# Performance work log

Hardware: AMD Instinct MI355X
Metric: run time of the kernel (lower is better)

The kernel has to match this reference:

```python
import jax, jax.numpy as jnp
import numpy as np

N = 100000   # nodes
C = 128      # in_channels
K = 32       # n_super_nodes
B = 16       # graphs in batch
TAU = 1.0
EPS = 1e-9
SPARSITY_W = 0.01
TEMPORAL_W = 0.1 * 5
COLLAPSE_W = 2.0


def setup_inputs() -> dict:
    key = jax.random.key(0)
    ks = jax.random.split(key, 8)
    x = jax.random.normal(ks[0], (N, C), dtype=jnp.float32)
    batch = jnp.sort(jax.random.randint(ks[1], (N,), 0, B)).astype(jnp.int64)
    pos = jax.random.normal(ks[2], (N, 2), dtype=jnp.float32)
    gumbel_u = jax.random.uniform(ks[3], (N, K), dtype=jnp.float32,
                                  minval=1e-6, maxval=1.0 - 1e-6)
    W1 = jax.random.normal(ks[4], (C, C), dtype=jnp.float32) / np.float32(np.sqrt(C))
    b1 = jnp.zeros((C,), jnp.float32)
    W2 = jax.random.normal(ks[5], (C, K), dtype=jnp.float32) / np.float32(np.sqrt(C))
    b2 = jnp.zeros((K,), jnp.float32)
    scaling = jnp.asarray(10.0, jnp.float32)
    active_mask = jnp.ones((K,), jnp.float32)
    return dict(x=x, batch=batch, pos=pos, gumbel_u=gumbel_u,
                W1=W1, b1=b1, W2=W2, b2=b2, scaling=scaling,
                active_mask=active_mask)


def reference(x, batch, pos, gumbel_u, W1, b1, W2, b2, scaling, active_mask):
    # assign MLP: Linear -> ReLU -> Linear, scaled
    h = jax.nn.relu(x @ W1 + b1)                      # [N, C]
    logits = (h @ W2 + b2) * scaling                  # [N, K]
    # eval-mode masking of inactive super-nodes (active_mask is a detached buffer)
    mask = jax.lax.stop_gradient(active_mask)[None, :]
    logits = jnp.where(mask == 0, -1e9, logits)
    # Gumbel-softmax (soft, hard=False) with explicit uniform noise
    g = -jnp.log(-jnp.log(gumbel_u + EPS) + EPS)
    s = jax.nn.softmax((logits + g) / TAU, axis=-1)   # [N, K]

    avg_s = s.mean(axis=0)                            # [K]
    entropy = -jnp.mean(jnp.sum(s * jnp.log(s + EPS), axis=1))
    uniform_p = 1.0 / K
    diversity = jnp.sum(uniform_p * jnp.log(uniform_p / (avg_s + EPS)))
    pruning = jnp.mean(jnp.abs(avg_s * (1.0 - active_mask)))
    sparsity = (jnp.sum(active_mask) / K) * SPARSITY_W
    temporal = jnp.asarray(0.0, s.dtype)  # prev_assignments=None

    # collapse prevention (common_losses approximation: normalized entropy
    # deficit + peak-mass penalty), scaled by collapse weight
    ent_avg = -jnp.sum(avg_s * jnp.log(avg_s + EPS))
    collapse = ((jnp.log(jnp.asarray(K, s.dtype)) - ent_avg)
                / jnp.log(jnp.asarray(K, s.dtype))
                + jax.nn.relu(jnp.max(avg_s) - 2.0 / K)) * COLLAPSE_W
    # balance (KL(avg_s || uniform))
    balance = jnp.sum(avg_s * jnp.log(avg_s * K + EPS))

    # spatial variance loss over column-normalized assignments
    s_sum = s.sum(axis=0, keepdims=True) + EPS        # [1, K]
    s_norm = s / s_sum                                # [N, K]
    mu = s_norm.T @ pos                               # [K, 2]
    pos_sq = jnp.sum(pos ** 2, axis=1, keepdims=True) # [N, 1]
    st_pos = s_norm.T @ pos                           # [K, 2]
    var = (s_norm.T @ pos_sq)[:, 0] - 2.0 * jnp.sum(mu * st_pos, axis=1) \
          + jnp.sum(mu ** 2, axis=1)
    spatial = var.mean()

    # per-graph super-node centroids via segment pooling
    sum_s_pos = jax.ops.segment_sum(pos[:, None, :] * s[:, :, None], batch,
                                    num_segments=B)   # [B, K, 2]
    sum_s = jax.ops.segment_sum(s, batch, num_segments=B)[:, :, None] + EPS
    super_node_mu = sum_s_pos / sum_s                 # [B, K, 2]

    # separation loss among centroids
    d = super_node_mu[:, :, None, :] - super_node_mu[:, None, :, :]
    dist_sq = jnp.sum(d ** 2, axis=-1)                # [B, K, K]
    eye = jnp.eye(K, dtype=s.dtype)[None]
    repulsion = 1.0 / (dist_sq + 1.0)
    separation = jnp.sum(repulsion * (1.0 - eye)) / (K * (K - 1) + EPS)

    # hierarchical pooling: out[b,k,c] = sum_{i in graph b} s[i,k] * x[i,c]
    x_expanded = x[:, None, :] * s[:, :, None]        # [N, K, C]
    out = jax.ops.segment_sum(x_expanded, batch, num_segments=B)  # [B, K, C]

    losses = jnp.stack([entropy, diversity, spatial, pruning, sparsity,
                        temporal * TEMPORAL_W, collapse, balance, separation])
    return out, s, super_node_mu, losses
```

## Files before the change

kernel.cpp:

```cpp
#include <hip/hip_runtime.h>
#include <math.h>

#define NN 100000
#define CC 128
#define KK 32
#define BG 16
#define EPSF 1e-9f

#define NTILES 1563

#define S_OFF 65536
#define MU_OFF 3265536
#define LOSS_OFF 3266560

#define WS_ENTARR 0
#define WS_STAT 2048
#define WS_FIRST 4096
#define WS_LAST 4112
#define WS_ZERO_FLOATS 4096

#define W1B_OFF_BYTES 16896
#define W2B_OFF_BYTES 49664
#define WS_PART_FLOAT 16384
#define WS_NEEDED_BYTES (65536ull + (unsigned long long)NTILES * 4096ull * 4ull)

typedef __attribute__((ext_vector_type(8))) _Float16 half8;
typedef __attribute__((ext_vector_type(4))) _Float16 half4v;
typedef __attribute__((ext_vector_type(4))) float float4v;

#define MFMAH(a, b, c) __builtin_amdgcn_mfma_f32_16x16x32_f16((a), (b), (c), 0, 0, 0)

__global__ __launch_bounds__(256) void k_prep(const float* __restrict__ W1,
                                              const float* __restrict__ W2,
                                              const int* __restrict__ batch,
                                              _Float16* __restrict__ wW1,
                                              _Float16* __restrict__ wW2,
                                              int* __restrict__ firstp,
                                              int* __restrict__ lastp,
                                              float* __restrict__ dout,
                                              float* __restrict__ ws) {
    int tid = blockIdx.x * 256 + threadIdx.x;

    float4 z4 = make_float4(0.f, 0.f, 0.f, 0.f);
#pragma unroll
    for (int i = 0; i < 4; ++i) ((float4*)dout)[tid + i * 4096] = z4;
    ws[tid] = 0.f;

    if (tid < 8 * 4 * 64) {
        int l = tid & 63, ks = (tid >> 6) & 3, nt = tid >> 8;
        int n = nt * 16 + (l & 15);
        int cb = ks * 32 + (l >> 4) * 8;
        half8 H;
#pragma unroll
        for (int j = 0; j < 8; ++j) H[j] = (_Float16)W1[(size_t)(cb + j) * CC + n];
        ((half8*)wW1)[(nt * 4 + ks) * 64 + l] = H;
    } else if (tid < 2048 + 512) {
        int t2 = tid - 2048;
        int l = t2 & 63, ks = (t2 >> 6) & 3, nt = t2 >> 8;
        int n = nt * 16 + (l & 15);
        int cb = ks * 32 + (l >> 4) * 8;
        half8 H;
#pragma unroll
        for (int j = 0; j < 8; ++j) H[j] = (_Float16)W2[(size_t)(cb + j) * KK + n];
        ((half8*)wW2)[(nt * 4 + ks) * 64 + l] = H;
    } else if (tid < 2560 + 16) {
        int b = tid - 2560;
        int lo = 0, hi = NN;
        while (lo < hi) { int mid = (lo + hi) >> 1; if (batch[mid] < b) lo = mid + 1; else hi = mid; }
        int lob = lo;
        lo = 0; hi = NN;
        while (lo < hi) { int mid = (lo + hi) >> 1; if (batch[mid] < b + 1) lo = mid + 1; else hi = mid; }
        int hib = (b == BG - 1) ? NTILES * 64 : lo;
        firstp[b] = (lob + 63) >> 6;
        lastp[b]  = (hib >> 6) - 1;
    }
}

__global__ __launch_bounds__(256, 4) void k_assign(
    const float* __restrict__ x, const int* __restrict__ batch,
    const float* __restrict__ pos, const float* __restrict__ gum,
    const float* __restrict__ b1, const float* __restrict__ b2,
    const float* __restrict__ scaling, const float* __restrict__ amask,
    const _Float16* __restrict__ wW1, const _Float16* __restrict__ wW2,
    float* __restrict__ dout, float* __restrict__ ws,
    float* __restrict__ part)
{
    __shared__ _Float16 xh[64][136];
    __shared__ _Float16 hb[64][136];
    __shared__ _Float16 st[32][72];
    __shared__ float lpx[64], lpy[64], lpsq[64];
    __shared__ int lbat[64];
    float* sbuf = (float*)&hb[0][0];

    const int t = threadIdx.x;
    const bool usep = (part != nullptr);
    const int orig = blockIdx.x;
    const int qq = NTILES >> 3, rr8 = NTILES & 7;
    const int xcd = orig & 7, sidx = orig >> 3;
    const int tile = (xcd < rr8 ? xcd * (qq + 1) : rr8 * (qq + 1) + (xcd - rr8) * qq) + sidx;
    const int n0 = tile * 64;

    const int l = t & 63;
    const int wv = __builtin_amdgcn_readfirstlane(t >> 6);
    const int li = l & 15;
    const int g16 = l >> 4;
    const int cc4 = (t & 31) * 4;
    const int nb = t >> 5;
    const int ca  = (2 * wv) * 16 + li;
    const int cb2 = (2 * wv + 1) * 16 + li;
    const int sk = t & 31, sch = t >> 5;

    const float scal = scaling[0];
    const float b2v0 = b2[li], b2v1 = b2[16 + li];
    const float am0 = amask[li], am1 = amask[16 + li];
    const float bv0 = b1[(2 * wv) * 16 + li];
    const float bv1 = b1[(2 * wv + 1) * 16 + li];

#pragma unroll
    for (int r = 0; r < 8; ++r) {
        int n = r * 8 + nb;
        int gn = n0 + n;
        float4 v = make_float4(0.f, 0.f, 0.f, 0.f);
        if (gn < NN) v = *(const float4*)(x + (size_t)gn * CC + cc4);
        *(half4v*)&xh[n][cc4] =
            (half4v){(_Float16)v.x, (_Float16)v.y, (_Float16)v.z, (_Float16)v.w};
    }
    if (t < 64) {
        int gn = n0 + t;
        float px = 0.f, py = 0.f; int bb = BG - 1;
        if (gn < NN) { px = pos[gn * 2]; py = pos[gn * 2 + 1]; bb = batch[gn]; }
        lpx[t] = px; lpy[t] = py; lpsq[t] = px * px + py * py; lbat[t] = bb;
    }

    float gu[8];
#pragma unroll
    for (int r2 = 0; r2 < 4; ++r2) {
        int gn = n0 + wv * 16 + g16 * 4 + r2;
        bool valid = gn < NN;
        gu[r2 * 2]     = valid ? gum[(size_t)gn * KK + li]      : 0.5f;
        gu[r2 * 2 + 1] = valid ? gum[(size_t)gn * KK + 16 + li] : 0.5f;
    }
    __syncthreads();

    float4v acc[4][2];
#pragma unroll
    for (int mt = 0; mt < 4; ++mt) {
        acc[mt][0] = (float4v){0.f, 0.f, 0.f, 0.f};
        acc[mt][1] = (float4v){0.f, 0.f, 0.f, 0.f};
    }
    const half8* W1B = (const half8*)wW1;
#pragma unroll
    for (int ks = 0; ks < 4; ++ks) {
        half8 bh0 = W1B[((2 * wv    ) * 4 + ks) * 64 + l];
        half8 bh1 = W1B[((2 * wv + 1) * 4 + ks) * 64 + l];
#pragma unroll
        for (int mt = 0; mt < 4; ++mt) {
            half8 ah = *(const half8*)&xh[mt * 16 + li][ks * 32 + g16 * 8];
            acc[mt][0] = MFMAH(ah, bh0, acc[mt][0]);
            acc[mt][1] = MFMAH(ah, bh1, acc[mt][1]);
        }
    }

#pragma unroll
    for (int mt = 0; mt < 4; ++mt) {
#pragma unroll
        for (int r2 = 0; r2 < 4; ++r2) {
            int row = mt * 16 + g16 * 4 + r2;
            hb[row][(2 * wv) * 16 + li]     = (_Float16)fmaxf(acc[mt][0][r2] + bv0, 0.f);
            hb[row][(2 * wv + 1) * 16 + li] = (_Float16)fmaxf(acc[mt][1][r2] + bv1, 0.f);
        }
    }
    __syncthreads();

    float4v acc2[2];
    acc2[0] = (float4v){0.f, 0.f, 0.f, 0.f};
    acc2[1] = (float4v){0.f, 0.f, 0.f, 0.f};
    const half8* W2B = (const half8*)wW2;
#pragma unroll
    for (int ks = 0; ks < 4; ++ks) {
        half8 ah = *(const half8*)&hb[wv * 16 + li][ks * 32 + g16 * 8];
        acc2[0] = MFMAH(ah, W2B[(0 * 4 + ks) * 64 + l], acc2[0]);
        acc2[1] = MFMAH(ah, W2B[(1 * 4 + ks) * 64 + l], acc2[1]);
    }

    float ep_acc = 0.f;
    float sr0[4], sr1[4];
#pragma unroll
    for (int r2 = 0; r2 < 4; ++r2) {
        int m = wv * 16 + g16 * 4 + r2;
        int gn = n0 + m;
        bool valid = gn < NN;
        float lg0 = (acc2[0][r2] + b2v0) * scal; if (am0 == 0.f) lg0 = -1e9f;
        float lg1 = (acc2[1][r2] + b2v1) * scal; if (am1 == 0.f) lg1 = -1e9f;
        float z0 = lg0 - __logf(-__logf(gu[r2 * 2] + EPSF) + EPSF);
        float z1 = lg1 - __logf(-__logf(gu[r2 * 2 + 1] + EPSF) + EPSF);
        float e0 = __expf(z0), e1 = __expf(z1);
        float sm = e0 + e1;
        sm += __shfl_xor(sm, 1);
        sm += __shfl_xor(sm, 2);
        sm += __shfl_xor(sm, 4);
        sm += __shfl_xor(sm, 8);
        float inv = 1.f / sm;
        float s0 = e0 * inv, s1 = e1 * inv;
        if (!valid) { s0 = 0.f; s1 = 0.f; }
        sr0[r2] = s0; sr1[r2] = s1;
        st[li][m] = (_Float16)s0;
        st[16 + li][m] = (_Float16)s1;
        ep_acc += s0 * __logf(s0 + EPSF) + s1 * __logf(s1 + EPSF);
    }
    __syncthreads();

    ep_acc += __shfl_xor(ep_acc, 1);
    ep_acc += __shfl_xor(ep_acc, 2);
    ep_acc += __shfl_xor(ep_acc, 4);
    ep_acc += __shfl_xor(ep_acc, 8);
    ep_acc += __shfl_xor(ep_acc, 16);
    ep_acc += __shfl_xor(ep_acc, 32);
    if (l == 0) sbuf[1024 + wv] = ep_acc;

    const int b0 = lbat[0], b63 = lbat[63];
    int cut = 64;
    if (b0 != b63) {
        for (int i = 1; i < 64; ++i) { if (lbat[i] != b0) { cut = i; break; } }
    }
    const int nseg = (b0 == b63) ? 1 : 2;

#pragma unroll 1
    for (int sg = 0; sg < nseg; ++sg) {
        const int lo = sg ? cut : 0;
        const int hi = sg ? 64 : cut;
        const int bb = sg ? b63 : b0;
        float prs = 0.f, ppx = 0.f, ppy = 0.f, psq = 0.f;
#pragma unroll
        for (int r = 0; r < 8; ++r) {
            int n = sch * 8 + r;
            if (n >= lo && n < hi) {
                float sv = (float)st[sk][n];
                prs += sv; ppx += sv * lpx[n]; ppy += sv * lpy[n]; psq += sv * lpsq[n];
            }
        }
        if (sg) __syncthreads();
        sbuf[(0 * 8 + sch) * 32 + sk] = prs;
        sbuf[(1 * 8 + sch) * 32 + sk] = ppx;
        sbuf[(2 * 8 + sch) * 32 + sk] = ppy;
        sbuf[(3 * 8 + sch) * 32 + sk] = psq;
        __syncthreads();
        if (t < 128) {
            int stat = t >> 5, k = t & 31;
            float a = 0.f;
#pragma unroll
            for (int c = 0; c < 8; ++c) a += sbuf[(stat * 8 + c) * 32 + k];
            atomicAdd(ws + WS_STAT + stat * 512 + bb * KK + k, a);
        }
    }

    if (t == 0) {
        ws[WS_ENTARR + orig] = sbuf[1024] + sbuf[1025] + sbuf[1026] + sbuf[1027];
    }

    float4v p00 = {0.f, 0.f, 0.f, 0.f}, p01 = p00, p10 = p00, p11 = p00;
    auto pool_flush = [&](int bb) {
        float* ob = dout + (size_t)bb * KK * CC;
#pragma unroll
        for (int r2 = 0; r2 < 4; ++r2) {
            int k0r = g16 * 4 + r2;
            atomicAdd(ob + k0r * CC + ca, p00[r2]);
            atomicAdd(ob + k0r * CC + cb2, p01[r2]);
            atomicAdd(ob + (16 + k0r) * CC + ca, p10[r2]);
            atomicAdd(ob + (16 + k0r) * CC + cb2, p11[r2]);
        }
        p00 = (float4v){0.f, 0.f, 0.f, 0.f}; p01 = p00; p10 = p00; p11 = p00;
    };
    if (b0 == b63) {
#pragma unroll
        for (int ksl = 0; ksl < 2; ++ksl) {
            half8 a0 = *(const half8*)&st[li][ksl * 32 + g16 * 8];
            half8 a1 = *(const half8*)&st[16 + li][ksl * 32 + g16 * 8];
            half8 v0, v1;
#pragma unroll
            for (int j = 0; j < 8; ++j) {
                int i = ksl * 32 + g16 * 8 + j;
                v0[j] = xh[i][ca];
                v1[j] = xh[i][cb2];
            }
            p00 = MFMAH(a0, v0, p00);
            p01 = MFMAH(a0, v1, p01);
            p10 = MFMAH(a1, v0, p10);
            p11 = MFMAH(a1, v1, p11);
        }
        if (usep) {
            float* pb = part + (size_t)tile * 4096;
#pragma unroll
            for (int r2 = 0; r2 < 4; ++r2) {
                int k0r = g16 * 4 + r2;
                pb[k0r * CC + ca]         = p00[r2];
                pb[k0r * CC + cb2]        = p01[r2];
                pb[(16 + k0r) * CC + ca]  = p10[r2];
                pb[(16 + k0r) * CC + cb2] = p11[r2];
            }
        } else {
            pool_flush(b0);
        }
    } else {
#pragma unroll 1
        for (int pass = 0; pass < 2; ++pass) {
            int lo = pass ? cut : 0;
            int hi = pass ? 64 : cut;
            int bb = pass ? b63 : b0;
#pragma unroll
            for (int ksl = 0; ksl < 2; ++ksl) {
                half8 a0, a1, v0, v1;
#pragma unroll
                for (int j = 0; j < 8; ++j) {
                    int i = ksl * 32 + g16 * 8 + j;
                    bool in = (i >= lo) && (i < hi);
                    a0[j] = in ? st[li][i] : (_Float16)0.f;
                    a1[j] = in ? st[16 + li][i] : (_Float16)0.f;
                    v0[j] = xh[i][ca];
                    v1[j] = xh[i][cb2];
                }
                p00 = MFMAH(a0, v0, p00);
                p01 = MFMAH(a0, v1, p01);
                p10 = MFMAH(a1, v0, p10);
                p11 = MFMAH(a1, v1, p11);
            }
            pool_flush(bb);
        }
    }

#pragma unroll
    for (int r2 = 0; r2 < 4; ++r2) {
        int gn = n0 + wv * 16 + g16 * 4 + r2;
        if (gn < NN) {
            dout[S_OFF + (size_t)gn * KK + li]      = sr0[r2];
            dout[S_OFF + (size_t)gn * KK + 16 + li] = sr1[r2];
        }
    }
}

__global__ __launch_bounds__(256) void k_reduce(const float* __restrict__ part,
                                                const int* __restrict__ firstp,
                                                const int* __restrict__ lastp,
                                                const float* __restrict__ ws,
                                                const float* __restrict__ amask,
                                                float* __restrict__ dout) {
    if (blockIdx.x < BG * 16 * 8) {
        if (part == nullptr) return;
        const int b   = blockIdx.x >> 7;
        const int elc = (blockIdx.x >> 3) & 15;
        const int sp  = blockIdx.x & 7;
        const int el  = elc * 256 + threadIdx.x;
        const int lo = firstp[b], hi = lastp[b];
        if (lo > hi) return;
        const int count = hi - lo + 1;
        const int per = (count + 7) >> 3;
        const int t0 = lo + sp * per;
        if (t0 > hi) return;
        int t1 = t0 + per - 1; if (t1 > hi) t1 = hi;
        float s0 = 0.f, s1 = 0.f;
        int tt = t0;
        for (; tt + 1 <= t1; tt += 2) {
            s0 += part[(size_t)tt * 4096 + el];
            s1 += part[(size_t)(tt + 1) * 4096 + el];
        }
        if (tt <= t1) s0 += part[(size_t)tt * 4096 + el];
        atomicAdd(dout + (size_t)b * 4096 + el, s0 + s1);
        return;
    }

    __shared__ float avg[32], csum[32], cpx[32], cpy[32], csq[32];
    __shared__ float lmu[16][32][2];
    __shared__ float red[4], ered[4];
    const int t = threadIdx.x;

    float esum = 0.f;
    for (int i = t; i < NTILES; i += 256) esum += ws[WS_ENTARR + i];
    esum += __shfl_xor(esum, 1);
    esum += __shfl_xor(esum, 2);
    esum += __shfl_xor(esum, 4);
    esum += __shfl_xor(esum, 8);
    esum += __shfl_xor(esum, 16);
    esum += __shfl_xor(esum, 32);
    if ((t & 63) == 0) ered[t >> 6] = esum;

    if (t < 32) {
        float a = 0.f, px = 0.f, py = 0.f, sq = 0.f;
        for (int b = 0; b < BG; ++b) {
            a  += ws[WS_STAT + 0 * 512 + b * KK + t];
            px += ws[WS_STAT + 1 * 512 + b * KK + t];
            py += ws[WS_STAT + 2 * 512 + b * KK + t];
            sq += ws[WS_STAT + 3 * 512 + b * KK + t];
        }
        csum[t] = a; cpx[t] = px; cpy[t] = py; csq[t] = sq;
        avg[t] = a / (float)NN;
    }
    for (int idx = t; idx < BG * KK; idx += 256) {
        float den = ws[WS_STAT + idx] + EPSF;
        float mx = ws[WS_STAT + 512 + idx] / den;
        float my = ws[WS_STAT + 1024 + idx] / den;
        int b = idx >> 5, k = idx & 31;
        lmu[b][k][0] = mx; lmu[b][k][1] = my;
        dout[MU_OFF + idx * 2] = mx;
        dout[MU_OFF + idx * 2 + 1] = my;
    }
    __syncthreads();
    float sep = 0.f;
    for (int idx = t; idx < BG * KK * KK; idx += 256) {
        int b = idx >> 10, k1 = (idx >> 5) & 31, k2 = idx & 31;
        if (k1 != k2) {
            float dx = lmu[b][k1][0] - lmu[b][k2][0];
            float dy = lmu[b][k1][1] - lmu[b][k2][1];
            sep += 1.f / (dx * dx + dy * dy + 1.f);
        }
    }
    for (int off = 32; off; off >>= 1) sep += __shfl_down(sep, off);
    if ((t & 63) == 0) red[t >> 6] = sep;
    __syncthreads();
    if (t == 0) {
        float sept = red[0] + red[1] + red[2] + red[3];
        float separation = sept / ((float)(KK * (KK - 1)) + EPSF);
        float entropy = -(ered[0] + ered[1] + ered[2] + ered[3]) / (float)NN;
        float diversity = 0.f, pruning = 0.f, msum = 0.f, entavg = 0.f, bal = 0.f, mxa = 0.f, spatial = 0.f;
        const float up = 1.f / (float)KK;
        for (int k = 0; k < KK; ++k) {
            float a = avg[k];
            diversity += up * logf(up / (a + EPSF));
            float mk = amask[k];
            pruning += fabsf(a * (1.f - mk));
            msum += mk;
            entavg -= a * logf(a + EPSF);
            bal += a * logf(a * (float)KK + EPSF);
            mxa = fmaxf(mxa, a);
            float den = csum[k] + EPSF;
            float mux = cpx[k] / den, muy = cpy[k] / den;
            spatial += csq[k] / den - (mux * mux + muy * muy);
        }
        pruning *= up;
        spatial *= up;
        const float lk = logf((float)KK);
        float collapse = ((lk - entavg) / lk + fmaxf(mxa - 2.f / (float)KK, 0.f)) * 2.0f;
        float sparsity = (msum / (float)KK) * 0.01f;
        dout[LOSS_OFF + 0] = entropy;
        dout[LOSS_OFF + 1] = diversity;
        dout[LOSS_OFF + 2] = spatial;
        dout[LOSS_OFF + 3] = pruning;
        dout[LOSS_OFF + 4] = sparsity;
        dout[LOSS_OFF + 5] = 0.f;
        dout[LOSS_OFF + 6] = collapse;
        dout[LOSS_OFF + 7] = bal;
        dout[LOSS_OFF + 8] = separation;
    }
}

extern "C" void kernel_launch(void* const* d_in, const int* in_sizes, int n_in,
                              void* d_out, int out_size, void* d_ws, size_t ws_size,
                              hipStream_t stream) {
    const float* x     = (const float*)d_in[0];
    const int*   batch = (const int*)d_in[1];
    const float* pos   = (const float*)d_in[2];
    const float* gum   = (const float*)d_in[3];
    const float* W1    = (const float*)d_in[4];
    const float* b1    = (const float*)d_in[5];
    const float* W2    = (const float*)d_in[6];
    const float* b2    = (const float*)d_in[7];
    const float* scal  = (const float*)d_in[8];
    const float* amask = (const float*)d_in[9];
    float* dout = (float*)d_out;
    float* ws   = (float*)d_ws;
    _Float16* wW1 = (_Float16*)((char*)d_ws + W1B_OFF_BYTES);
    _Float16* wW2 = (_Float16*)((char*)d_ws + W2B_OFF_BYTES);
    int* firstp = (int*)(ws + WS_FIRST);
    int* lastp  = (int*)(ws + WS_LAST);
    const bool usep = (ws_size >= (size_t)WS_NEEDED_BYTES);
    float* partp = usep ? (ws + WS_PART_FLOAT) : nullptr;

    k_prep<<<16, 256, 0, stream>>>(W1, W2, batch, wW1, wW2, firstp, lastp, dout, ws);
    k_assign<<<NTILES, 256, 0, stream>>>(x, batch, pos, gum, b1, b2,
                                         scal, amask, wW1, wW2, dout, ws, partp);
    k_reduce<<<BG * 16 * 8 + 1, 256, 0, stream>>>(partp, firstp, lastp, ws, amask, dout);
}
```

Measured before the change: 72.12 us.

## Replace per-tile pooling partials with per-XCD atomic replicas reduced in final kernel

Previously each single-graph tile wrote a full 4096-float partial to a large workspace array (about 25 MB), and the reduce kernel summed those partials per graph using first/last tile indices from a binary search. Now every tile atomically adds into one of 8 per-XCD replicas of the B×K×C output held in workspace. The reduce kernel sums the 8 replicas. This removes the large partial write and read traffic and the binary-search setup, at the cost of more global atomics, which are kept XCD-local to limit cross-die contention. The prep kernel now zeroes the 2 MB of replicas instead of the output.

```diff
diff --git a/kernel.cpp b/kernel.cpp
--- a/kernel.cpp
+++ b/kernel.cpp
@@ -15,14 +15,11 @@
 
 #define WS_ENTARR 0
 #define WS_STAT 2048
-#define WS_FIRST 4096
-#define WS_LAST 4112
-#define WS_ZERO_FLOATS 4096
 
 #define W1B_OFF_BYTES 16896
 #define W2B_OFF_BYTES 49664
-#define WS_PART_FLOAT 16384
-#define WS_NEEDED_BYTES (65536ull + (unsigned long long)NTILES * 4096ull * 4ull)
+#define WS_POOL 16384
+#define WS_POOL_STRIDE (BG * 4096)
 
 typedef __attribute__((ext_vector_type(8))) _Float16 half8;
 typedef __attribute__((ext_vector_type(4))) _Float16 half4v;
@@ -32,19 +29,16 @@
 
 __global__ __launch_bounds__(256) void k_prep(const float* __restrict__ W1,
                                               const float* __restrict__ W2,
-                                              const int* __restrict__ batch,
                                               _Float16* __restrict__ wW1,
                                               _Float16* __restrict__ wW2,
-                                              int* __restrict__ firstp,
-                                              int* __restrict__ lastp,
-                                              float* __restrict__ dout,
                                               float* __restrict__ ws) {
     int tid = blockIdx.x * 256 + threadIdx.x;
 
+    ws[tid] = 0.f;
     float4 z4 = make_float4(0.f, 0.f, 0.f, 0.f);
-#pragma unroll
-    for (int i = 0; i < 4; ++i) ((float4*)dout)[tid + i * 4096] = z4;
-    ws[tid] = 0.f;
+    float4* pr = (float4*)(ws + WS_POOL);
+#pragma unroll
+    for (int i = 0; i < 32; ++i) pr[tid + i * 4096] = z4;
 
     if (tid < 8 * 4 * 64) {
         int l = tid & 63, ks = (tid >> 6) & 3, nt = tid >> 8;
@@ -63,16 +57,6 @@
 #pragma unroll
         for (int j = 0; j < 8; ++j) H[j] = (_Float16)W2[(size_t)(cb + j) * KK + n];
         ((half8*)wW2)[(nt * 4 + ks) * 64 + l] = H;
-    } else if (tid < 2560 + 16) {
-        int b = tid - 2560;
-        int lo = 0, hi = NN;
-        while (lo < hi) { int mid = (lo + hi) >> 1; if (batch[mid] < b) lo = mid + 1; else hi = mid; }
-        int lob = lo;
-        lo = 0; hi = NN;
-        while (lo < hi) { int mid = (lo + hi) >> 1; if (batch[mid] < b + 1) lo = mid + 1; else hi = mid; }
-        int hib = (b == BG - 1) ? NTILES * 64 : lo;
-        firstp[b] = (lob + 63) >> 6;
-        lastp[b]  = (hib >> 6) - 1;
     }
 }
 
@@ -82,8 +66,7 @@
     const float* __restrict__ b1, const float* __restrict__ b2,
     const float* __restrict__ scaling, const float* __restrict__ amask,
     const _Float16* __restrict__ wW1, const _Float16* __restrict__ wW2,
-    float* __restrict__ dout, float* __restrict__ ws,
-    float* __restrict__ part)
+    float* __restrict__ dout, float* __restrict__ ws)
 {
     __shared__ _Float16 xh[64][136];
     __shared__ _Float16 hb[64][136];
@@ -93,7 +76,6 @@
     float* sbuf = (float*)&hb[0][0];
 
     const int t = threadIdx.x;
-    const bool usep = (part != nullptr);
     const int orig = blockIdx.x;
     const int qq = NTILES >> 3, rr8 = NTILES & 7;
     const int xcd = orig & 7, sidx = orig >> 3;
@@ -109,6 +91,7 @@
     const int ca  = (2 * wv) * 16 + li;
     const int cb2 = (2 * wv + 1) * 16 + li;
     const int sk = t & 31, sch = t >> 5;
+    float* rep = ws + WS_POOL + xcd * WS_POOL_STRIDE;
 
     const float scal = scaling[0];
     const float b2v0 = b2[li], b2v1 = b2[16 + li];
@@ -260,7 +243,7 @@
 
     float4v p00 = {0.f, 0.f, 0.f, 0.f}, p01 = p00, p10 = p00, p11 = p00;
     auto pool_flush = [&](int bb) {
-        float* ob = dout + (size_t)bb * KK * CC;
+        float* ob = rep + bb * 4096;
 #pragma unroll
         for (int r2 = 0; r2 < 4; ++r2) {
             int k0r = g16 * 4 + r2;
@@ -288,19 +271,7 @@
             p10 = MFMAH(a1, v0, p10);
             p11 = MFMAH(a1, v1, p11);
         }
-        if (usep) {
-            float* pb = part + (size_t)tile * 4096;
-#pragma unroll
-            for (int r2 = 0; r2 < 4; ++r2) {
-                int k0r = g16 * 4 + r2;
-                pb[k0r * CC + ca]         = p00[r2];
-                pb[k0r * CC + cb2]        = p01[r2];
-                pb[(16 + k0r) * CC + ca]  = p10[r2];
-                pb[(16 + k0r) * CC + cb2] = p11[r2];
-            }
-        } else {
-            pool_flush(b0);
-        }
+        pool_flush(b0);
     } else {
 #pragma unroll 1
         for (int pass = 0; pass < 2; ++pass) {
@@ -338,33 +309,17 @@
     }
 }
 
-__global__ __launch_bounds__(256) void k_reduce(const float* __restrict__ part,
-                                                const int* __restrict__ firstp,
-                                                const int* __restrict__ lastp,
-                                                const float* __restrict__ ws,
+__global__ __launch_bounds__(256) void k_reduce(const float* __restrict__ ws,
                                                 const float* __restrict__ amask,
                                                 float* __restrict__ dout) {
-    if (blockIdx.x < BG * 16 * 8) {
-        if (part == nullptr) return;
-        const int b   = blockIdx.x >> 7;
-        const int elc = (blockIdx.x >> 3) & 15;
-        const int sp  = blockIdx.x & 7;
-        const int el  = elc * 256 + threadIdx.x;
-        const int lo = firstp[b], hi = lastp[b];
-        if (lo > hi) return;
-        const int count = hi - lo + 1;
-        const int per = (count + 7) >> 3;
-        const int t0 = lo + sp * per;
-        if (t0 > hi) return;
-        int t1 = t0 + per - 1; if (t1 > hi) t1 = hi;
-        float s0 = 0.f, s1 = 0.f;
-        int tt = t0;
-        for (; tt + 1 <= t1; tt += 2) {
-            s0 += part[(size_t)tt * 4096 + el];
-            s1 += part[(size_t)(tt + 1) * 4096 + el];
-        }
-        if (tt <= t1) s0 += part[(size_t)tt * 4096 + el];
-        atomicAdd(dout + (size_t)b * 4096 + el, s0 + s1);
+    if (blockIdx.x < 256) {
+        const int b = blockIdx.x >> 4;
+        const int el = (blockIdx.x & 15) * 256 + threadIdx.x;
+        const float* pr = ws + WS_POOL;
+        float s = 0.f;
+#pragma unroll
+        for (int r = 0; r < 8; ++r) s += pr[r * WS_POOL_STRIDE + b * 4096 + el];
+        dout[(size_t)b * 4096 + el] = s;
         return;
     }
 
@@ -469,13 +424,9 @@
     float* ws   = (float*)d_ws;
     _Float16* wW1 = (_Float16*)((char*)d_ws + W1B_OFF_BYTES);
     _Float16* wW2 = (_Float16*)((char*)d_ws + W2B_OFF_BYTES);
-    int* firstp = (int*)(ws + WS_FIRST);
-    int* lastp  = (int*)(ws + WS_LAST);
-    const bool usep = (ws_size >= (size_t)WS_NEEDED_BYTES);
-    float* partp = usep ? (ws + WS_PART_FLOAT) : nullptr;
-
-    k_prep<<<16, 256, 0, stream>>>(W1, W2, batch, wW1, wW2, firstp, lastp, dout, ws);
+
+    k_prep<<<16, 256, 0, stream>>>(W1, W2, wW1, wW2, ws);
     k_assign<<<NTILES, 256, 0, stream>>>(x, batch, pos, gum, b1, b2,
-                                         scal, amask, wW1, wW2, dout, ws, partp);
-    k_reduce<<<BG * 16 * 8 + 1, 256, 0, stream>>>(partp, firstp, lastp, ws, amask, dout);
+                                         scal, amask, wW1, wW2, dout, ws);
+    k_reduce<<<257, 256, 0, stream>>>(ws, amask, dout);
 }
```

Result: slower. 75.88 us (+5.2%).
